# Performance work log

Hardware: AMD Instinct MI355X
Metric: run time of the kernel (lower is better)

## Reference

```python
import jax, jax.numpy as jnp
import numpy as np

EPS = 1e-6


def setup_inputs() -> dict:
    key = jax.random.key(0)
    k1, k2, k3, k4 = jax.random.split(key, 4)
    B, L, H, E = 16, 4096, 8, 64
    return {
        "queries": jax.random.normal(k1, (B, L, H, E), dtype=jnp.float32),
        "keys": jax.random.normal(k2, (B, L, H, E), dtype=jnp.float32),
        "values": jax.random.normal(k3, (B, L, H, E), dtype=jnp.float32),
        "attn_mask": jnp.ones((1,), dtype=bool),
        "gamma": jax.random.uniform(k4, (1,), dtype=jnp.float32),
    }


def reference(queries, keys, values, attn_mask, gamma):
    # Faithful to the original: keys/values/attn_mask are unused; Q=K=V=queries.
    B, L, H, E = queries.shape
    HE = H * E
    V = queries.reshape(B, L, HE)              # raw values [B, L, HE]
    # l2_norm: normalize over dim=-2 (the L axis)
    Qn = V / jnp.linalg.norm(V, axis=-2, keepdims=True)   # [B, L, HE]
    Kt = jnp.swapaxes(Qn, -1, -2)              # K = l2_norm(K).permute -> [B, HE, L]
    # tailor_sum: 1 / (HE + sum_n Kt[b,n,l] * (sum_l' Qn[b,l',n] + eps))  -> [B, L]
    q_colsum = jnp.sum(Qn, axis=-2) + EPS      # [B, HE]
    tailor = 1.0 / (HE + jnp.einsum('bnl,bn->bl', Kt, q_colsum))  # [B, L]
    # value_sum over L, broadcast to [B, L, HE]
    value_sum = jnp.sum(V, axis=-2)            # [B, HE]
    # (V @ K) @ Q == V @ (K @ Q): use the linear-complexity [HE,HE] inner matrix
    KQ = jnp.einsum('bnl,blm->bnm', Kt, Qn)    # [B, HE, HE]
    part = jnp.einsum('bln,bnm->blm', V, KQ)   # [B, L, HE]
    matrix_sum = value_sum[:, None, :] + part  # [B, L, HE]
    weight_value = (matrix_sum * tailor[:, :, None]).reshape(B, L, H, E)
    return queries + gamma * weight_value
```

## Files before the change

### kernel.cpp

```cpp
#include <hip/hip_runtime.h>

#define EPS 1e-6f
#define LL 4096
#define HE 512

typedef __attribute__((ext_vector_type(8))) short short8;
typedef __attribute__((ext_vector_type(4))) float f32x4;

__device__ __forceinline__ unsigned short f2bf(float f) {
    union { float f; unsigned u; } v; v.f = f;
    unsigned r = v.u + 0x7FFFu + ((v.u >> 16) & 1u);
    return (unsigned short)(r >> 16);
}
__device__ __forceinline__ float bf2f(unsigned short s) {
    union { unsigned u; float f; } v; v.u = ((unsigned)s) << 16;
    return v.f;
}
__device__ __forceinline__ void gl16(const unsigned short* g, unsigned short* l) {
    __builtin_amdgcn_global_load_lds(
        (const __attribute__((address_space(1))) unsigned int*)(const void*)g,
        (__attribute__((address_space(3))) unsigned int*)(void*)l,
        16, 0, 0);
}

__global__ __launch_bounds__(256) void k1_fused(const float* __restrict__ q,
        unsigned short* __restrict__ Vt, unsigned short* __restrict__ Vb,
        float* __restrict__ ps, float* __restrict__ pq, int bofs, int pstride) {
    __shared__ unsigned short lds[64][65];
    int blk = blockIdx.x;
    int b = blk >> 9, lt = (blk >> 3) & 63, nt = blk & 7;
    int gb = bofs + b;
    int t = threadIdx.x;
    int row = t >> 4, col = (t & 15) << 2;
    const float* base = q + ((size_t)gb * LL + lt * 64) * HE + nt * 64;
    unsigned short* vbb = Vb + ((size_t)b * LL + lt * 64) * HE + nt * 64;
    #pragma unroll
    for (int i = 0; i < 4; i++) {
        int l = row + i * 16;
        float4 v = *(const float4*)(base + (size_t)l * HE + col);
        ushort4 w;
        w.x = f2bf(v.x); w.y = f2bf(v.y); w.z = f2bf(v.z); w.w = f2bf(v.w);
        lds[col+0][l] = w.x; lds[col+1][l] = w.y;
        lds[col+2][l] = w.z; lds[col+3][l] = w.w;
        *(ushort4*)(vbb + (size_t)l * HE + col) = w;
    }
    __syncthreads();
    unsigned short* ob = Vt + ((size_t)b * HE + nt * 64) * LL + lt * 64;
    #pragma unroll
    for (int i = 0; i < 4; i++) {
        int n = row + i * 16;
        ushort4 w;
        w.x = lds[n][col+0]; w.y = lds[n][col+1];
        w.z = lds[n][col+2]; w.w = lds[n][col+3];
        *(ushort4*)(ob + (size_t)n * LL + col) = w;
        float x0 = bf2f(w.x), x1 = bf2f(w.y), x2 = bf2f(w.z), x3 = bf2f(w.w);
        float s = x0 + x1 + x2 + x3;
        float qq = x0*x0 + x1*x1 + x2*x2 + x3*x3;
        s += __shfl_xor(s, 1);  qq += __shfl_xor(qq, 1);
        s += __shfl_xor(s, 2);  qq += __shfl_xor(qq, 2);
        s += __shfl_xor(s, 4);  qq += __shfl_xor(qq, 4);
        s += __shfl_xor(s, 8);  qq += __shfl_xor(qq, 8);
        if ((t & 15) == 0) {
            int idx = lt * pstride + b * 512 + nt * 64 + n;
            ps[idx] = s;
            pq[idx] = qq;
        }
    }
}

__global__ __launch_bounds__(256) void k2_reduce(const float* __restrict__ ps,
        const float* __restrict__ pq, float* __restrict__ sumV,
        float* __restrict__ cvec, float* __restrict__ invn, int bofs, int pstride) {
    int i = blockIdx.x * 256 + threadIdx.x;
    float s = 0.f, qq = 0.f;
    #pragma unroll 8
    for (int lt = 0; lt < 64; lt++) {
        s  += ps[(size_t)lt * pstride + i];
        qq += pq[(size_t)lt * pstride + i];
    }
    int o = bofs * HE + i;
    float inv = 1.0f / sqrtf(qq);
    sumV[o] = s;
    invn[o] = inv;
    cvec[o] = (s * inv + EPS) * inv;
}

__global__ __launch_bounds__(256) void k3_dvec(const unsigned short* __restrict__ Vb,
        const float* __restrict__ cvec, float* __restrict__ dvec, int bofs) {
    int blk = blockIdx.x;
    int b = blk >> 7, lblk = blk & 127;
    int t = threadIdx.x;
    int lloc = t >> 3, j = t & 7;
    int l = lblk * 32 + lloc;
    const unsigned short* rowp = Vb + ((size_t)b * LL + l) * HE + j * 64;
    const float* cp = cvec + (bofs + b) * HE + j * 64;
    float d = 0.f;
    #pragma unroll
    for (int g = 0; g < 8; g++) {
        short8 v = *(const short8*)(rowp + g * 8);
        float4 c0 = *(const float4*)(cp + g * 8);
        float4 c1 = *(const float4*)(cp + g * 8 + 4);
        d += bf2f((unsigned short)v[0]) * c0.x + bf2f((unsigned short)v[1]) * c0.y
           + bf2f((unsigned short)v[2]) * c0.z + bf2f((unsigned short)v[3]) * c0.w
           + bf2f((unsigned short)v[4]) * c1.x + bf2f((unsigned short)v[5]) * c1.y
           + bf2f((unsigned short)v[6]) * c1.z + bf2f((unsigned short)v[7]) * c1.w;
    }
    d += __shfl_xor(d, 1); d += __shfl_xor(d, 2); d += __shfl_xor(d, 4);
    if (j == 0) dvec[(size_t)(bofs + b) * LL + l] = d;
}

__global__ __launch_bounds__(256) void k4_gram(const unsigned short* __restrict__ Vt,
        unsigned short* __restrict__ Gp) {
    __shared__ __attribute__((aligned(16))) unsigned short la[2][128][64];
    __shared__ __attribute__((aligned(16))) unsigned short lb[2][128][64];
    int cpx = gridDim.x >> 3;
    int blk = ((int)blockIdx.x & 7) * cpx + ((int)blockIdx.x >> 3);
    int b = blk / 80;
    int rem = blk - b * 80;
    int pair = rem >> 3, split = rem & 7;
    int nt = (pair < 4) ? 0 : (pair < 7) ? 1 : (pair < 9) ? 2 : 3;
    int off = (nt * (9 - nt)) >> 1;
    int mt = nt + pair - off;
    bool diag = (nt == mt);
    int N0 = nt * 128, M0 = mt * 128;
    int t = threadIdx.x;
    int w = t >> 6, lane = t & 63;
    int wr = w >> 1, wc = w & 1;
    int rl = lane >> 3;
    int cl = ((lane & 7) ^ rl) << 3;
    int lr = lane & 15, q4 = lane >> 4;
    int ch0 = (q4 ^ (lane & 7)) << 3;
    const unsigned short* pa = Vt + ((size_t)b * HE + N0) * LL + split * 512;
    const unsigned short* pb = Vt + ((size_t)b * HE + M0) * LL + split * 512;
    f32x4 acc[4][4] = {};

#define STAGE4(B, KB) do { \
    int _k0 = (KB) * 64; \
    _Pragma("unroll") \
    for (int p = 0; p < 4; p++) { \
        int r0 = p * 32 + w * 8; \
        gl16(pa + (size_t)(r0 + rl) * LL + _k0 + cl, &la[B][r0][0]); \
        if (!diag) gl16(pb + (size_t)(r0 + rl) * LL + _k0 + cl, &lb[B][r0][0]); \
    } } while (0)

    STAGE4(0, 0);
    #pragma unroll
    for (int kb = 0; kb < 8; kb++) {
        int cur = kb & 1;
        if (kb < 7) {
            STAGE4(cur ^ 1, kb + 1);
            if (diag) { asm volatile("s_waitcnt vmcnt(4)" ::: "memory"); }
            else      { asm volatile("s_waitcnt vmcnt(8)" ::: "memory"); }
        } else {
            asm volatile("s_waitcnt vmcnt(0)" ::: "memory");
        }
        __builtin_amdgcn_s_barrier();
        const unsigned short (*A)[64] = la[cur];
        const unsigned short (*Bp)[64] = diag ? la[cur] : lb[cur];
        #pragma unroll
        for (int ks = 0; ks < 2; ks++) {
            int colA = ch0 ^ (ks << 5);
            short8 af[4], bfr[4];
            #pragma unroll
            for (int i = 0; i < 4; i++)
                af[i] = *(const short8*)&A[wr*64 + i*16 + lr][colA];
            #pragma unroll
            for (int j = 0; j < 4; j++)
                bfr[j] = *(const short8*)&Bp[wc*64 + j*16 + lr][colA];
            #pragma unroll
            for (int i = 0; i < 4; i++)
                #pragma unroll
                for (int j = 0; j < 4; j++)
                    acc[i][j] = __builtin_amdgcn_mfma_f32_16x16x32_bf16(af[i], bfr[j], acc[i][j], 0, 0, 0);
        }
        __builtin_amdgcn_s_barrier();
    }
#undef STAGE4
    size_t tbase = ((size_t)(b * 10 + pair) * 8 + split) * 16384;
    #pragma unroll
    for (int i = 0; i < 4; i++) {
        int nb = wr*64 + i*16 + q4*4;
        #pragma unroll
        for (int j = 0; j < 4; j++) {
            int ml = wc*64 + j*16 + lr;
            ushort4 wv;
            wv.x = f2bf(acc[i][j][0]); wv.y = f2bf(acc[i][j][1]);
            wv.z = f2bf(acc[i][j][2]); wv.w = f2bf(acc[i][j][3]);
            *(ushort4*)&Gp[tbase + (size_t)ml * 128 + nb] = wv;
        }
    }
}

__global__ __launch_bounds__(256) void k5_reduce(const unsigned short* __restrict__ Gp,
        const float* __restrict__ invn, unsigned short* __restrict__ KQb, int bofs) {
    __shared__ unsigned short lds_t[128][130];
    int blk = blockIdx.x;
    int b = blk / 10, pair = blk % 10;
    int nt = (pair < 4) ? 0 : (pair < 7) ? 1 : (pair < 9) ? 2 : 3;
    int off = (nt * (9 - nt)) >> 1;
    int mt = nt + pair - off;
    int N0 = nt * 128, M0 = mt * 128;
    int t = threadIdx.x;
    const unsigned short* gp = Gp + ((size_t)(b * 10 + pair) * 8) * 16384;
    const float* inb = invn + (size_t)(bofs + b) * HE;
    #pragma unroll 2
    for (int e = 0; e < 32; e++) {
        int idx = e * 512 + t * 2;
        int ml = idx >> 7, nl = idx & 127;
        float s0 = 0.f, s1 = 0.f;
        #pragma unroll
        for (int sp = 0; sp < 8; sp++) {
            unsigned g2 = *(const unsigned*)&gp[(size_t)sp * 16384 + idx];
            s0 += bf2f((unsigned short)(g2 & 0xFFFF));
            s1 += bf2f((unsigned short)(g2 >> 16));
        }
        float im = inb[M0 + ml];
        ushort2 v;
        v.x = f2bf(s0 * inb[N0 + nl] * im);
        v.y = f2bf(s1 * inb[N0 + nl + 1] * im);
        *(ushort2*)&KQb[((size_t)b * HE + M0 + ml) * HE + N0 + nl] = v;
        *(ushort2*)&lds_t[ml][nl] = v;
    }
    __syncthreads();
    #pragma unroll 2
    for (int e = 0; e < 32; e++) {
        int idx = e * 512 + t * 2;
        int nl = idx >> 7, ml = idx & 127;
        ushort2 v;
        v.x = lds_t[ml][nl];
        v.y = lds_t[ml + 1][nl];
        *(ushort2*)&KQb[((size_t)b * HE + N0 + nl) * HE + M0 + ml] = v;
    }
}

__global__ __launch_bounds__(256) void k6_part(const unsigned short* __restrict__ KQb,
        const unsigned short* __restrict__ Vb, const float* __restrict__ dvec,
        const float* __restrict__ sumV, const float* __restrict__ gamma,
        float* __restrict__ out, int bofs) {
    __shared__ __attribute__((aligned(16))) unsigned short la[2][128][64];
    __shared__ __attribute__((aligned(16))) unsigned short lb[2][128][64];
    int cpx = gridDim.x >> 3;
    int blk = ((int)blockIdx.x & 7) * cpx + ((int)blockIdx.x >> 3);
    int b = blk >> 7, mt = (blk >> 5) & 3, lt = blk & 31;
    int gb = bofs + b;
    int M0 = mt * 128, L0 = lt * 128;
    int t = threadIdx.x;
    int w = t >> 6, lane = t & 63;
    int wr = w >> 1, wc = w & 1;
    int rl = lane >> 3;
    int cl = ((lane & 7) ^ rl) << 3;
    int lr = lane & 15, q4 = lane >> 4;
    int ch0 = (q4 ^ (lane & 7)) << 3;
    const unsigned short* pa = KQb + ((size_t)b * HE + M0) * HE;
    const unsigned short* pb = Vb + ((size_t)b * LL + L0) * HE;
    float gma = gamma[0];
    f32x4 acc[4][4] = {};

#define STAGE6(B, KB) do { \
    int _k0 = (KB) * 64; \
    _Pragma("unroll") \
    for (int p = 0; p < 4; p++) { \
        int r0 = p * 32 + w * 8; \
        gl16(pa + (size_t)(r0 + rl) * HE + _k0 + cl, &la[B][r0][0]); \
        gl16(pb + (size_t)(r0 + rl) * HE + _k0 + cl, &lb[B][r0][0]); \
    } } while (0)

    STAGE6(0, 0);
    #pragma unroll
    for (int kb = 0; kb < 8; kb++) {
        int cur = kb & 1;
        if (kb < 7) {
            STAGE6(cur ^ 1, kb + 1);
            asm volatile("s_waitcnt vmcnt(8)" ::: "memory");
        } else {
            asm volatile("s_waitcnt vmcnt(0)" ::: "memory");
        }
        __builtin_amdgcn_s_barrier();
        #pragma unroll
        for (int ks = 0; ks < 2; ks++) {
            int colA = ch0 ^ (ks << 5);
            short8 af[4], bfr[4];
            #pragma unroll
            for (int i = 0; i < 4; i++)
                af[i] = *(const short8*)&la[cur][wr*64 + i*16 + lr][colA];
            #pragma unroll
            for (int j = 0; j < 4; j++)
                bfr[j] = *(const short8*)&lb[cur][wc*64 + j*16 + lr][colA];
            #pragma unroll
            for (int i = 0; i < 4; i++)
                #pragma unroll
                for (int j = 0; j < 4; j++)
                    acc[i][j] = __builtin_amdgcn_mfma_f32_16x16x32_bf16(af[i], bfr[j], acc[i][j], 0, 0, 0);
        }
        __builtin_amdgcn_s_barrier();
    }
#undef STAGE6
    #pragma unroll
    for (int j = 0; j < 4; j++) {
        int lglob = L0 + wc*64 + j*16 + lr;
        float dt = dvec[(size_t)gb * LL + lglob];
        float tailor = 1.0f / (512.0f + dt);
        #pragma unroll
        for (int i = 0; i < 4; i++) {
            int m4 = M0 + wr*64 + i*16 + q4*4;
            size_t ofs = ((size_t)gb * LL + lglob) * HE + m4;
            ushort4 rv = *(const ushort4*)(Vb + ((size_t)b * LL + lglob) * HE + m4);
            float4 vs = *(const float4*)(sumV + (size_t)gb * HE + m4);
            float4 o;
            o.x = bf2f(rv.x) + gma * (vs.x + acc[i][j][0]) * tailor;
            o.y = bf2f(rv.y) + gma * (vs.y + acc[i][j][1]) * tailor;
            o.z = bf2f(rv.z) + gma * (vs.z + acc[i][j][2]) * tailor;
            o.w = bf2f(rv.w) + gma * (vs.w + acc[i][j][3]) * tailor;
            *(float4*)(out + ofs) = o;
        }
    }
}

extern "C" void kernel_launch(void* const* d_in, const int* in_sizes, int n_in,
                              void* d_out, int out_size, void* d_ws, size_t ws_size,
                              hipStream_t stream) {
    const float* q     = (const float*)d_in[0];
    const float* gamma = (const float*)d_in[4];
    float* out = (float*)d_out;
    char* ws = (char*)d_ws;
    float* sumV  = (float*)(ws);
    float* cvec  = (float*)(ws + 65536);
    float* invn  = (float*)(ws + 98304);
    float* dvec  = (float*)(ws + 131072);

    if (ws_size >= 190000000ull) {
        unsigned short* KQb = (unsigned short*)(ws + 524288);
        unsigned short* Vt  = (unsigned short*)(ws + 8912896);
        unsigned short* Vb  = (unsigned short*)(ws + 76021760);
        unsigned short* Gp  = (unsigned short*)(ws + 143130624);
        float* ps = (float*)(ws + 185073664);
        float* pq = (float*)(ws + 187170816);
        k1_fused <<<8192, 256, 0, stream>>>(q, Vt, Vb, ps, pq, 0, 8192);
        k2_reduce<<<32,   256, 0, stream>>>(ps, pq, sumV, cvec, invn, 0, 8192);
        k3_dvec  <<<2048, 256, 0, stream>>>(Vb, cvec, dvec, 0);
        k4_gram  <<<1280, 256, 0, stream>>>(Vt, Gp);
        k5_reduce<<<160,  256, 0, stream>>>(Gp, invn, KQb, 0);
        k6_part  <<<2048, 256, 0, stream>>>(KQb, Vb, dvec, sumV, gamma, out, 0);
    } else {
        unsigned short* KQb = (unsigned short*)(ws + 524288);
        unsigned short* Vt  = (unsigned short*)(ws + 524288 + 4194304);
        unsigned short* Vb  = (unsigned short*)(ws + 524288 + 4194304 + 33554432);
        unsigned short* Gp = (unsigned short*)((float*)d_out + 16777216);
        float* ps = (float*)d_out + 22020096;
        float* pq = ps + 262144;
        for (int h = 0; h < 2; h++) {
            int bofs = h * 8;
            k1_fused <<<4096, 256, 0, stream>>>(q, Vt, Vb, ps, pq, bofs, 4096);
            k2_reduce<<<16,   256, 0, stream>>>(ps, pq, sumV, cvec, invn, bofs, 4096);
            k3_dvec  <<<1024, 256, 0, stream>>>(Vb, cvec, dvec, bofs);
            k4_gram  <<<640,  256, 0, stream>>>(Vt, Gp);
            k5_reduce<<<80,   256, 0, stream>>>(Gp, invn, KQb, bofs);
            k6_part  <<<1024, 256, 0, stream>>>(KQb, Vb, dvec, sumV, gamma, out, bofs);
        }
    }
}
```

Measured before the change: 199.5 us.

## Drop transposed Vt copy; gram kernel transposes Vb tiles in registers to LDS

The first kernel no longer writes a transposed bf16 copy of the input. It streams rows into Vb and accumulates column sums and sums of squares per block. The gram kernel now loads row-major Vb tiles into registers and writes them transposed into swizzled LDS, replacing the async global-to-LDS loads and double buffering with a single buffer plus register prefetch. The small-workspace fallback path is removed, so the code assumes a large workspace. This saves one full-size write and its later read, but risks a slower gram kernel because loads now stage through registers and the LDS pipeline has only one buffer.

```diff
diff --git a/kernel.cpp b/kernel.cpp
--- a/kernel.cpp
+++ b/kernel.cpp
@@ -23,77 +23,75 @@
         16, 0, 0);
 }
 
-__global__ __launch_bounds__(256) void k1_fused(const float* __restrict__ q,
-        unsigned short* __restrict__ Vt, unsigned short* __restrict__ Vb,
-        float* __restrict__ ps, float* __restrict__ pq, int bofs, int pstride) {
-    __shared__ unsigned short lds[64][65];
+__global__ __launch_bounds__(256) void k1_stream(const float* __restrict__ q,
+        unsigned short* __restrict__ Vb, float* __restrict__ ps,
+        float* __restrict__ pq) {
+    __shared__ float lds_s[4][512];
+    __shared__ float lds_q[4][512];
     int blk = blockIdx.x;
-    int b = blk >> 9, lt = (blk >> 3) & 63, nt = blk & 7;
-    int gb = bofs + b;
-    int t = threadIdx.x;
-    int row = t >> 4, col = (t & 15) << 2;
-    const float* base = q + ((size_t)gb * LL + lt * 64) * HE + nt * 64;
-    unsigned short* vbb = Vb + ((size_t)b * LL + lt * 64) * HE + nt * 64;
-    #pragma unroll
-    for (int i = 0; i < 4; i++) {
-        int l = row + i * 16;
-        float4 v = *(const float4*)(base + (size_t)l * HE + col);
-        ushort4 w;
-        w.x = f2bf(v.x); w.y = f2bf(v.y); w.z = f2bf(v.z); w.w = f2bf(v.w);
-        lds[col+0][l] = w.x; lds[col+1][l] = w.y;
-        lds[col+2][l] = w.z; lds[col+3][l] = w.w;
-        *(ushort4*)(vbb + (size_t)l * HE + col) = w;
+    int b = blk >> 6, lt = blk & 63;
+    int t = threadIdx.x;
+    int oct = t & 63, w = t >> 6;
+    size_t rowbase = (size_t)b * LL + lt * 64 + w * 16;
+    const float* qb = q + rowbase * HE + oct * 8;
+    unsigned short* vb = Vb + rowbase * HE + oct * 8;
+    float s[8] = {}, qq[8] = {};
+    #pragma unroll
+    for (int r = 0; r < 16; r++) {
+        float4 v0 = *(const float4*)(qb + (size_t)r * HE);
+        float4 v1 = *(const float4*)(qb + (size_t)r * HE + 4);
+        unsigned short e[8] = {f2bf(v0.x), f2bf(v0.y), f2bf(v0.z), f2bf(v0.w),
+                               f2bf(v1.x), f2bf(v1.y), f2bf(v1.z), f2bf(v1.w)};
+        short8 w8;
+        #pragma unroll
+        for (int c = 0; c < 8; c++) {
+            w8[c] = (short)e[c];
+            float x = bf2f(e[c]);
+            s[c] += x; qq[c] += x * x;
+        }
+        *(short8*)(vb + (size_t)r * HE) = w8;
+    }
+    #pragma unroll
+    for (int c = 0; c < 8; c++) {
+        lds_s[w][oct * 8 + c] = s[c];
+        lds_q[w][oct * 8 + c] = qq[c];
     }
     __syncthreads();
-    unsigned short* ob = Vt + ((size_t)b * HE + nt * 64) * LL + lt * 64;
-    #pragma unroll
-    for (int i = 0; i < 4; i++) {
-        int n = row + i * 16;
-        ushort4 w;
-        w.x = lds[n][col+0]; w.y = lds[n][col+1];
-        w.z = lds[n][col+2]; w.w = lds[n][col+3];
-        *(ushort4*)(ob + (size_t)n * LL + col) = w;
-        float x0 = bf2f(w.x), x1 = bf2f(w.y), x2 = bf2f(w.z), x3 = bf2f(w.w);
-        float s = x0 + x1 + x2 + x3;
-        float qq = x0*x0 + x1*x1 + x2*x2 + x3*x3;
-        s += __shfl_xor(s, 1);  qq += __shfl_xor(qq, 1);
-        s += __shfl_xor(s, 2);  qq += __shfl_xor(qq, 2);
-        s += __shfl_xor(s, 4);  qq += __shfl_xor(qq, 4);
-        s += __shfl_xor(s, 8);  qq += __shfl_xor(qq, 8);
-        if ((t & 15) == 0) {
-            int idx = lt * pstride + b * 512 + nt * 64 + n;
-            ps[idx] = s;
-            pq[idx] = qq;
-        }
+    #pragma unroll
+    for (int h = 0; h < 2; h++) {
+        int col = h * 256 + t;
+        float ss = lds_s[0][col] + lds_s[1][col] + lds_s[2][col] + lds_s[3][col];
+        float sq = lds_q[0][col] + lds_q[1][col] + lds_q[2][col] + lds_q[3][col];
+        ps[(size_t)lt * 8192 + b * 512 + col] = ss;
+        pq[(size_t)lt * 8192 + b * 512 + col] = sq;
     }
 }
 
 __global__ __launch_bounds__(256) void k2_reduce(const float* __restrict__ ps,
         const float* __restrict__ pq, float* __restrict__ sumV,
-        float* __restrict__ cvec, float* __restrict__ invn, int bofs, int pstride) {
+        float* __restrict__ cvec, float* __restrict__ invn) {
     int i = blockIdx.x * 256 + threadIdx.x;
     float s = 0.f, qq = 0.f;
     #pragma unroll 8
     for (int lt = 0; lt < 64; lt++) {
-        s  += ps[(size_t)lt * pstride + i];
-        qq += pq[(size_t)lt * pstride + i];
-    }
-    int o = bofs * HE + i;
+        s  += ps[(size_t)lt * 8192 + i];
+        qq += pq[(size_t)lt * 8192 + i];
+    }
     float inv = 1.0f / sqrtf(qq);
-    sumV[o] = s;
-    invn[o] = inv;
-    cvec[o] = (s * inv + EPS) * inv;
+    sumV[i] = s;
+    invn[i] = inv;
+    cvec[i] = (s * inv + EPS) * inv;
 }
 
 __global__ __launch_bounds__(256) void k3_dvec(const unsigned short* __restrict__ Vb,
-        const float* __restrict__ cvec, float* __restrict__ dvec, int bofs) {
+        const float* __restrict__ cvec, float* __restrict__ dvec) {
     int blk = blockIdx.x;
     int b = blk >> 7, lblk = blk & 127;
     int t = threadIdx.x;
     int lloc = t >> 3, j = t & 7;
     int l = lblk * 32 + lloc;
     const unsigned short* rowp = Vb + ((size_t)b * LL + l) * HE + j * 64;
-    const float* cp = cvec + (bofs + b) * HE + j * 64;
+    const float* cp = cvec + b * HE + j * 64;
     float d = 0.f;
     #pragma unroll
     for (int g = 0; g < 8; g++) {
@@ -106,13 +104,13 @@
            + bf2f((unsigned short)v[6]) * c1.z + bf2f((unsigned short)v[7]) * c1.w;
     }
     d += __shfl_xor(d, 1); d += __shfl_xor(d, 2); d += __shfl_xor(d, 4);
-    if (j == 0) dvec[(size_t)(bofs + b) * LL + l] = d;
-}
-
-__global__ __launch_bounds__(256) void k4_gram(const unsigned short* __restrict__ Vt,
+    if (j == 0) dvec[(size_t)b * LL + l] = d;
+}
+
+__global__ __launch_bounds__(256) void k4_gram(const unsigned short* __restrict__ Vb,
         unsigned short* __restrict__ Gp) {
-    __shared__ __attribute__((aligned(16))) unsigned short la[2][128][64];
-    __shared__ __attribute__((aligned(16))) unsigned short lb[2][128][64];
+    __shared__ __attribute__((aligned(16))) unsigned short lt_a[128][72];
+    __shared__ __attribute__((aligned(16))) unsigned short lt_b[128][72];
     int cpx = gridDim.x >> 3;
     int blk = ((int)blockIdx.x & 7) * cpx + ((int)blockIdx.x >> 3);
     int b = blk / 80;
@@ -126,63 +124,78 @@
     int t = threadIdx.x;
     int w = t >> 6, lane = t & 63;
     int wr = w >> 1, wc = w & 1;
-    int rl = lane >> 3;
-    int cl = ((lane & 7) ^ rl) << 3;
     int lr = lane & 15, q4 = lane >> 4;
-    int ch0 = (q4 ^ (lane & 7)) << 3;
-    const unsigned short* pa = Vt + ((size_t)b * HE + N0) * LL + split * 512;
-    const unsigned short* pb = Vt + ((size_t)b * HE + M0) * LL + split * 512;
+    int oct = t & 15;
+    int l0 = (t >> 4) * 4;
+    int lp = l0 ^ (8 * (oct & 7));
+    const unsigned short* pa = Vb + ((size_t)b * LL + split * 512) * HE + N0 + oct * 8;
+    const unsigned short* pb = Vb + ((size_t)b * LL + split * 512) * HE + M0 + oct * 8;
     f32x4 acc[4][4] = {};
-
-#define STAGE4(B, KB) do { \
-    int _k0 = (KB) * 64; \
+    short8 ra[4], rb[4];
+
+#define K4LOAD(KB) do { \
     _Pragma("unroll") \
-    for (int p = 0; p < 4; p++) { \
-        int r0 = p * 32 + w * 8; \
-        gl16(pa + (size_t)(r0 + rl) * LL + _k0 + cl, &la[B][r0][0]); \
-        if (!diag) gl16(pb + (size_t)(r0 + rl) * LL + _k0 + cl, &lb[B][r0][0]); \
+    for (int r = 0; r < 4; r++) { \
+        size_t ro = (size_t)((KB) * 64 + l0 + r) * HE; \
+        ra[r] = *(const short8*)(pa + ro); \
+        if (!diag) rb[r] = *(const short8*)(pb + ro); \
     } } while (0)
 
-    STAGE4(0, 0);
+#define K4WRITE() do { \
+    _Pragma("unroll") \
+    for (int c = 0; c < 8; c++) { \
+        uint2 da; \
+        da.x = (unsigned)(unsigned short)ra[0][c] | ((unsigned)(unsigned short)ra[1][c] << 16); \
+        da.y = (unsigned)(unsigned short)ra[2][c] | ((unsigned)(unsigned short)ra[3][c] << 16); \
+        *(uint2*)&lt_a[oct * 8 + c][lp] = da; \
+        if (!diag) { \
+            uint2 db; \
+            db.x = (unsigned)(unsigned short)rb[0][c] | ((unsigned)(unsigned short)rb[1][c] << 16); \
+            db.y = (unsigned)(unsigned short)rb[2][c] | ((unsigned)(unsigned short)rb[3][c] << 16); \
+            *(uint2*)&lt_b[oct * 8 + c][lp] = db; \
+        } \
+    } } while (0)
+
+    K4LOAD(0);
     #pragma unroll
     for (int kb = 0; kb < 8; kb++) {
-        int cur = kb & 1;
-        if (kb < 7) {
-            STAGE4(cur ^ 1, kb + 1);
-            if (diag) { asm volatile("s_waitcnt vmcnt(4)" ::: "memory"); }
-            else      { asm volatile("s_waitcnt vmcnt(8)" ::: "memory"); }
-        } else {
-            asm volatile("s_waitcnt vmcnt(0)" ::: "memory");
-        }
+        if (kb) __builtin_amdgcn_s_barrier();
+        K4WRITE();
+        if (kb < 7) K4LOAD(kb + 1);
+        asm volatile("s_waitcnt lgkmcnt(0)" ::: "memory");
         __builtin_amdgcn_s_barrier();
-        const unsigned short (*A)[64] = la[cur];
-        const unsigned short (*Bp)[64] = diag ? la[cur] : lb[cur];
         #pragma unroll
         for (int ks = 0; ks < 2; ks++) {
-            int colA = ch0 ^ (ks << 5);
             short8 af[4], bfr[4];
             #pragma unroll
-            for (int i = 0; i < 4; i++)
-                af[i] = *(const short8*)&A[wr*64 + i*16 + lr][colA];
-            #pragma unroll
-            for (int j = 0; j < 4; j++)
-                bfr[j] = *(const short8*)&Bp[wc*64 + j*16 + lr][colA];
+            for (int i = 0; i < 4; i++) {
+                int row = wr * 64 + i * 16 + lr;
+                int col = (ks * 32 + q4 * 8) ^ (8 * ((2 * i + (lr >> 3)) & 7));
+                af[i] = *(const short8*)&lt_a[row][col];
+            }
+            #pragma unroll
+            for (int j = 0; j < 4; j++) {
+                int row = wc * 64 + j * 16 + lr;
+                int col = (ks * 32 + q4 * 8) ^ (8 * ((2 * j + (lr >> 3)) & 7));
+                bfr[j] = diag ? *(const short8*)&lt_a[row][col]
+                              : *(const short8*)&lt_b[row][col];
+            }
             #pragma unroll
             for (int i = 0; i < 4; i++)
                 #pragma unroll
                 for (int j = 0; j < 4; j++)
                     acc[i][j] = __builtin_amdgcn_mfma_f32_16x16x32_bf16(af[i], bfr[j], acc[i][j], 0, 0, 0);
         }
-        __builtin_amdgcn_s_barrier();
-    }
-#undef STAGE4
+    }
+#undef K4LOAD
+#undef K4WRITE
     size_t tbase = ((size_t)(b * 10 + pair) * 8 + split) * 16384;
     #pragma unroll
     for (int i = 0; i < 4; i++) {
-        int nb = wr*64 + i*16 + q4*4;
+        int nb = wr * 64 + i * 16 + q4 * 4;
         #pragma unroll
         for (int j = 0; j < 4; j++) {
-            int ml = wc*64 + j*16 + lr;
+            int ml = wc * 64 + j * 16 + lr;
             ushort4 wv;
             wv.x = f2bf(acc[i][j][0]); wv.y = f2bf(acc[i][j][1]);
             wv.z = f2bf(acc[i][j][2]); wv.w = f2bf(acc[i][j][3]);
@@ -192,7 +205,7 @@
 }
 
 __global__ __launch_bounds__(256) void k5_reduce(const unsigned short* __restrict__ Gp,
-        const float* __restrict__ invn, unsigned short* __restrict__ KQb, int bofs) {
+        const float* __restrict__ invn, unsigned short* __restrict__ KQb) {
     __shared__ unsigned short lds_t[128][130];
     int blk = blockIdx.x;
     int b = blk / 10, pair = blk % 10;
@@ -202,7 +215,7 @@
     int N0 = nt * 128, M0 = mt * 128;
     int t = threadIdx.x;
     const unsigned short* gp = Gp + ((size_t)(b * 10 + pair) * 8) * 16384;
-    const float* inb = invn + (size_t)(bofs + b) * HE;
+    const float* inb = invn + (size_t)b * HE;
     #pragma unroll 2
     for (int e = 0; e < 32; e++) {
         int idx = e * 512 + t * 2;
@@ -236,13 +249,12 @@
 __global__ __launch_bounds__(256) void k6_part(const unsigned short* __restrict__ KQb,
         const unsigned short* __restrict__ Vb, const float* __restrict__ dvec,
         const float* __restrict__ sumV, const float* __restrict__ gamma,
-        float* __restrict__ out, int bofs) {
+        float* __restrict__ out) {
     __shared__ __attribute__((aligned(16))) unsigned short la[2][128][64];
     __shared__ __attribute__((aligned(16))) unsigned short lb[2][128][64];
     int cpx = gridDim.x >> 3;
     int blk = ((int)blockIdx.x & 7) * cpx + ((int)blockIdx.x >> 3);
     int b = blk >> 7, mt = (blk >> 5) & 3, lt = blk & 31;
-    int gb = bofs + b;
     int M0 = mt * 128, L0 = lt * 128;
     int t = threadIdx.x;
     int w = t >> 6, lane = t & 63;
@@ -298,14 +310,14 @@
     #pragma unroll
     for (int j = 0; j < 4; j++) {
         int lglob = L0 + wc*64 + j*16 + lr;
-        float dt = dvec[(size_t)gb * LL + lglob];
+        float dt = dvec[(size_t)b * LL + lglob];
         float tailor = 1.0f / (512.0f + dt);
         #pragma unroll
         for (int i = 0; i < 4; i++) {
             int m4 = M0 + wr*64 + i*16 + q4*4;
-            size_t ofs = ((size_t)gb * LL + lglob) * HE + m4;
+            size_t ofs = ((size_t)b * LL + lglob) * HE + m4;
             ushort4 rv = *(const ushort4*)(Vb + ((size_t)b * LL + lglob) * HE + m4);
-            float4 vs = *(const float4*)(sumV + (size_t)gb * HE + m4);
+            float4 vs = *(const float4*)(sumV + (size_t)b * HE + m4);
             float4 o;
             o.x = bf2f(rv.x) + gma * (vs.x + acc[i][j][0]) * tailor;
             o.y = bf2f(rv.y) + gma * (vs.y + acc[i][j][1]) * tailor;
@@ -327,35 +339,16 @@
     float* cvec  = (float*)(ws + 65536);
     float* invn  = (float*)(ws + 98304);
     float* dvec  = (float*)(ws + 131072);
-
-    if (ws_size >= 190000000ull) {
-        unsigned short* KQb = (unsigned short*)(ws + 524288);
-        unsigned short* Vt  = (unsigned short*)(ws + 8912896);
-        unsigned short* Vb  = (unsigned short*)(ws + 76021760);
-        unsigned short* Gp  = (unsigned short*)(ws + 143130624);
-        float* ps = (float*)(ws + 185073664);
-        float* pq = (float*)(ws + 187170816);
-        k1_fused <<<8192, 256, 0, stream>>>(q, Vt, Vb, ps, pq, 0, 8192);
-        k2_reduce<<<32,   256, 0, stream>>>(ps, pq, sumV, cvec, invn, 0, 8192);
-        k3_dvec  <<<2048, 256, 0, stream>>>(Vb, cvec, dvec, 0);
-        k4_gram  <<<1280, 256, 0, stream>>>(Vt, Gp);
-        k5_reduce<<<160,  256, 0, stream>>>(Gp, invn, KQb, 0);
-        k6_part  <<<2048, 256, 0, stream>>>(KQb, Vb, dvec, sumV, gamma, out, 0);
-    } else {
-        unsigned short* KQb = (unsigned short*)(ws + 524288);
-        unsigned short* Vt  = (unsigned short*)(ws + 524288 + 4194304);
-        unsigned short* Vb  = (unsigned short*)(ws + 524288 + 4194304 + 33554432);
-        unsigned short* Gp = (unsigned short*)((float*)d_out + 16777216);
-        float* ps = (float*)d_out + 22020096;
-        float* pq = ps + 262144;
-        for (int h = 0; h < 2; h++) {
-            int bofs = h * 8;
-            k1_fused <<<4096, 256, 0, stream>>>(q, Vt, Vb, ps, pq, bofs, 4096);
-            k2_reduce<<<16,   256, 0, stream>>>(ps, pq, sumV, cvec, invn, bofs, 4096);
-            k3_dvec  <<<1024, 256, 0, stream>>>(Vb, cvec, dvec, bofs);
-            k4_gram  <<<640,  256, 0, stream>>>(Vt, Gp);
-            k5_reduce<<<80,   256, 0, stream>>>(Gp, invn, KQb, bofs);
-            k6_part  <<<1024, 256, 0, stream>>>(KQb, Vb, dvec, sumV, gamma, out, bofs);
-        }
-    }
-}
+    unsigned short* KQb = (unsigned short*)(ws + 524288);
+    unsigned short* Vb  = (unsigned short*)(ws + 8912896);
+    unsigned short* Gp  = (unsigned short*)(ws + 76021760);
+    float* ps = (float*)(ws + 117964800);
+    float* pq = (float*)(ws + 120061952);
+
+    k1_stream<<<1024, 256, 0, stream>>>(q, Vb, ps, pq);
+    k2_reduce<<<32,   256, 0, stream>>>(ps, pq, sumV, cvec, invn);
+    k3_dvec  <<<2048, 256, 0, stream>>>(Vb, cvec, dvec);
+    k4_gram  <<<1280, 256, 0, stream>>>(Vb, Gp);
+    k5_reduce<<<160,  256, 0, stream>>>(Gp, invn, KQb);
+    k6_part  <<<2048, 256, 0, stream>>>(KQb, Vb, dvec, sumV, gamma, out);
+}
```

Result: slower. 203.7 us (+2.1%).
